# Optimization experiments

Measured on AMD Instinct MI355X. Metric: run time of the kernel, lower is better.

## Reference

```python
import math
import jax, jax.numpy as jnp
import numpy as np

N_EMBD = 1024
N_HEAD = 16
B, T = 2, 2048


def _heads(t):
    # (B, T, D) -> (B, H, T, hd)
    b, s, d = t.shape
    return t.reshape(b, s, N_HEAD, d // N_HEAD).transpose(0, 2, 1, 3)


def setup_inputs() -> dict:
    key = jax.random.key(0)
    ks = jax.random.split(key, 7)
    D = N_EMBD
    s = 0.02
    return {
        "x": jax.random.normal(ks[0], (B, T, D), dtype=jnp.float32),
        "w_attn": jax.random.normal(ks[1], (2 * D, D), dtype=jnp.float32) * s,
        "b_attn": jnp.zeros((2 * D,), dtype=jnp.float32),
        "w_k2": jax.random.normal(ks[2], (D, D), dtype=jnp.float32) * s,
        "b_k2": jnp.zeros((D,), dtype=jnp.float32),
        "w_proj": jax.random.normal(ks[3], (D, D), dtype=jnp.float32) * s,
        "b_proj": jnp.zeros((D,), dtype=jnp.float32),
    }


def reference(x, w_attn, b_attn, w_k2, b_k2, w_proj, b_proj):
    b, t, d = x.shape
    hd = d // N_HEAD
    scale = 1.0 / math.sqrt(hd)

    # QKV projections: q,k from c_attn; v is raw x reshaped into heads
    qk = x @ w_attn.T + b_attn
    q, k = jnp.split(qk, 2, axis=-1)
    q, k, v = _heads(q), _heads(k), _heads(x)  # (B,H,T,hd)

    # AR branch: standard causal softmax attention
    scores = jnp.einsum("bhqd,bhkd->bhqk", q, k) * scale
    causal = jnp.tril(jnp.ones((t, t), dtype=bool))
    scores = jnp.where(causal, scores, -jnp.inf)
    y_ar = jnp.einsum("bhqk,bhkd->bhqd", jax.nn.softmax(scores, axis=-1), v)

    # MA branch on one-step residuals e_t = v_{t+1} - y_ar_t
    e = v[:, :, 1:, :] - y_ar[:, :, :-1, :]           # (B,H,T-1,hd)
    q2 = q[:, :, 1:, :]
    k2 = _heads(x[:, :-1] @ w_k2.T + b_k2)            # (B,H,T-1,hd)

    qa = -jax.nn.leaky_relu(-q2 * scale, negative_slope=0.02)  # ma_q_activation
    ka = jax.nn.sigmoid((k2 * scale) * 0.02)                   # ma_k_activation, k=0.02

    ma = jnp.einsum("bhqd,bhkd->bhqk", qa, ka)        # (B,H,T-1,T-1), no softmax
    ma = jnp.where(jnp.tril(jnp.ones((t - 1, t - 1), dtype=bool)), ma, 0.0)
    y_ma = jnp.einsum("bhqk,bhkd->bhqd", ma, e)
    y_ma = jnp.concatenate([jnp.zeros_like(y_ma[:, :, :1, :]), y_ma], axis=2)

    def merge(z):  # (B,H,T,hd) -> (B,T,D)
        return z.transpose(0, 2, 1, 3).reshape(b, t, d)

    out = (merge(y_ar) @ w_proj.T + b_proj) + (merge(y_ma) @ w_proj.T + b_proj)
    return out
```

## Files before the change

### kernel.cpp

```cpp
#include <hip/hip_runtime.h>
#include <hip/hip_bf16.h>
#include <math.h>

#define BB  2
#define TT  2048
#define DDE 1024
#define NHH 16
#define HDD 64

typedef __bf16 bf16_t;
typedef __attribute__((ext_vector_type(8))) __bf16 bf16x8;
typedef __attribute__((ext_vector_type(4))) __bf16 bf16x4;
typedef __attribute__((ext_vector_type(4))) float  f32x4;

#define MFMA(a, b, c) __builtin_amdgcn_mfma_f32_16x16x32_bf16((a), (b), (c), 0, 0, 0)

#define WAIT_VM6()   asm volatile("s_waitcnt vmcnt(6)" ::: "memory")
#define WAIT_VM4()   asm volatile("s_waitcnt vmcnt(4)" ::: "memory")
#define WAIT_VM0()   asm volatile("s_waitcnt vmcnt(0)" ::: "memory")
#define WAIT_LGKM0() asm volatile("s_waitcnt lgkmcnt(0)" ::: "memory")

__device__ inline void wg_barrier() {
    __builtin_amdgcn_sched_barrier(0);
    __builtin_amdgcn_s_barrier();
    __builtin_amdgcn_sched_barrier(0);
}

__device__ inline unsigned int cvtpk(float a, float b) {
    unsigned int r;
    asm("v_cvt_pk_bf16_f32 %0, %1, %2" : "=v"(r) : "v"(a), "v"(b));
    return r;
}

__device__ inline float fexp2(float x) {
    float r;
    asm("v_exp_f32 %0, %1" : "=v"(r) : "v"(x));
    return r;
}

__device__ inline void pl16swap(unsigned int &a, unsigned int &b) {
    asm("v_permlane16_swap_b32 %0, %1" : "+v"(a), "+v"(b));
}

__device__ inline void gll16(const bf16_t* g, unsigned short* l) {
    __builtin_amdgcn_global_load_lds(
        (const __attribute__((address_space(1))) void*)g,
        (__attribute__((address_space(3))) void*)l, 16, 0, 0);
}

template<int ROWS, int NW = 4>
__device__ inline void stage_tile(const bf16_t* g0, size_t gstride,
                                  unsigned short* lds, int wave, int lane)
{
    const int r8 = lane >> 3;
    const int ck = (lane & 7) ^ r8;
    constexpr int RW = ROWS / NW;
    const bf16_t* g = g0 + (size_t)(wave * RW + r8) * gstride + ck * 8;
    unsigned short* l = lds + wave * RW * 64 + lane * 8;
    #pragma unroll
    for (int i = 0; i < RW / 8; ++i)
        gll16(g + (size_t)(i * 8) * gstride, l + i * 512);
}

__global__ __launch_bounds__(256) void cvt_all(
    const float* __restrict__ x, const float* __restrict__ wa,
    const float* __restrict__ wk, const float* __restrict__ wp,
    bf16_t* __restrict__ out)
{
    const size_t NX  = (size_t)BB*TT*DDE;
    const size_t NWA = (size_t)2*DDE*DDE;
    const size_t NW  = (size_t)DDE*DDE;
    const size_t e = ((size_t)blockIdx.x * 256 + threadIdx.x) * 4;
    const float* src;
    if (e < NX)                 src = x  + e;
    else if (e < NX + NWA)      src = wa + (e - NX);
    else if (e < NX + NWA + NW) src = wk + (e - NX - NWA);
    else                        src = wp + (e - NX - NWA - NW);
    float4 v = *(const float4*)src;
    bf16x4 o;
    o[0] = (bf16_t)v.x; o[1] = (bf16_t)v.y;
    o[2] = (bf16_t)v.z; o[3] = (bf16_t)v.w;
    *(bf16x4*)(out + e) = o;
}

__global__ __launch_bounds__(256) void transpose_head(
    const bf16_t* __restrict__ src, bf16_t* __restrict__ dst)
{
    const int t0 = blockIdx.x * 64, h = blockIdx.y, b = blockIdx.z;
    const int tid = threadIdx.x;
    __shared__ __align__(16) bf16_t tile[64 * 64];

    #pragma unroll
    for (int it = 0; it < 2; ++it) {
        const int t = it * 32 + (tid >> 3);
        const int cw = tid & 7;
        const int slot = (cw + (t >> 3)) & 7;
        bf16x8 v = *(const bf16x8*)(src + (size_t)(b*TT + t0 + t)*DDE + h*HDD + cw*8);
        *(bf16x8*)(tile + t*64 + slot*8) = v;
    }
    __syncthreads();
    const int bh = b * NHH + h;
    #pragma unroll
    for (int it = 0; it < 2; ++it) {
        const int d = it * 32 + (tid >> 3);
        const int co = tid & 7;
        const int slot = ((d >> 3) + co) & 7;
        bf16x8 o;
        #pragma unroll
        for (int j = 0; j < 8; ++j)
            o[j] = tile[(co*8 + j)*64 + slot*8 + (d & 7)];
        *(bf16x8*)(dst + (size_t)(bh*64 + d)*TT + t0 + co*8) = o;
    }
}

__global__ __launch_bounds__(256) void build_etg(
    const bf16_t* __restrict__ yarb, const bf16_t* __restrict__ xb,
    bf16_t* __restrict__ etg)
{
    const int t0 = blockIdx.x * 64, h = blockIdx.y, b = blockIdx.z;
    const int tid = threadIdx.x;
    const int bh = b * NHH + h;
    __shared__ __align__(16) bf16_t tile[64 * 64];

    #pragma unroll
    for (int it = 0; it < 2; ++it) {
        const int t = it * 32 + (tid >> 3);
        const int cw = tid & 7;
        const int slot = (cw + (t >> 3)) & 7;
        const int tg = t0 + t;
        bf16x8 ev;
        if (tg == 0) {
            #pragma unroll
            for (int u = 0; u < 8; ++u) ev[u] = (bf16_t)0.f;
        } else {
            bf16x8 xv = *(const bf16x8*)(xb   + (size_t)(b*TT + tg)*DDE + h*HDD + cw*8);
            bf16x8 nv = *(const bf16x8*)(yarb + (size_t)(b*TT + tg - 1)*DDE + h*HDD + cw*8);
            #pragma unroll
            for (int u = 0; u < 8; ++u)
                ev[u] = (bf16_t)((float)xv[u] - (float)nv[u]);
        }
        *(bf16x8*)(tile + t*64 + slot*8) = ev;
    }
    __syncthreads();
    #pragma unroll
    for (int it = 0; it < 2; ++it) {
        const int d = it * 32 + (tid >> 3);
        const int co = tid & 7;
        const int slot = ((d >> 3) + co) & 7;
        bf16x8 o;
        #pragma unroll
        for (int j = 0; j < 8; ++j)
            o[j] = tile[(co*8 + j)*64 + slot*8 + (d & 7)];
        *(bf16x8*)(etg + (size_t)(bh*64 + d)*TT + t0 + co*8) = o;
    }
}

__global__ __launch_bounds__(256) void gemm_qkk2(
    const bf16_t* __restrict__ A, const bf16_t* __restrict__ wab,
    const bf16_t* __restrict__ wkb, const float* __restrict__ b_attn,
    const float* __restrict__ b_k2, bf16_t* __restrict__ qkb,
    bf16_t* __restrict__ qab, bf16_t* __restrict__ kcs)
{
    __shared__ __align__(16) unsigned short As[2][64 * 64];
    __shared__ __align__(16) unsigned short Bs[2][128 * 64];
    const int tid  = threadIdx.x;
    const int wave = tid >> 6, lane = tid & 63;
    const int l15  = lane & 15, quad = lane >> 4;
    const int lid = (int)blockIdx.y * 24 + (int)blockIdx.x;
    const int s   = (lid & 7) * 192 + (lid >> 3);
    const int bm = (s / 24) * 64, bn = (s % 24) * 128;
    const int wm = (wave & 1) * 32, wn = (wave >> 1) * 64;
    const int region = bn >> 10;
    const int K = DDE;
    constexpr int NST = DDE / 64;

    const bf16_t* W = (region < 2) ? wab + (size_t)bn * K
                                   : wkb + (size_t)(bn - 2048) * K;
    const float* bp = (region < 2) ? b_attn + bn : b_k2 + (bn - 2048);
    const bf16_t* Ab = A + (size_t)bm * K;

    f32x4 acc[2][4];
    #pragma unroll
    for (int i = 0; i < 2; ++i)
        #pragma unroll
        for (int j = 0; j < 4; ++j) acc[i][j] = (f32x4)0.f;

    stage_tile<64>(Ab, K, As[0], wave, lane);
    stage_tile<128>(W,  K, Bs[0], wave, lane);
    stage_tile<64>(Ab + 64, K, As[1], wave, lane);
    stage_tile<128>(W  + 64, K, Bs[1], wave, lane);

    for (int t = 0; t < NST; ++t) {
        if (t + 1 < NST) WAIT_VM6(); else WAIT_VM0();
        wg_barrier();
        const unsigned short* Ac = As[t & 1];
        const unsigned short* Bc = Bs[t & 1];
        bf16x8 af[2][2], bfr[4][2];
        #pragma unroll
        for (int mt = 0; mt < 2; ++mt)
            #pragma unroll
            for (int kh = 0; kh < 2; ++kh)
                af[mt][kh] = *(const bf16x8*)(Ac + (wm + mt*16 + l15)*64
                                              + (((kh*4 + quad) ^ (l15 & 7))*8));
        #pragma unroll
        for (int nt = 0; nt < 4; ++nt)
            #pragma unroll
            for (int kh = 0; kh < 2; ++kh)
                bfr[nt][kh] = *(const bf16x8*)(Bc + (wn + nt*16 + l15)*64
                                               + (((kh*4 + quad) ^ (l15 & 7))*8));
        __builtin_amdgcn_s_setprio(1);
        #pragma unroll
        for (int mt = 0; mt < 2; ++mt)
            #pragma unroll
            for (int nt = 0; nt < 4; ++nt) {
                acc[mt][nt] = MFMA(af[mt][0], bfr[nt][0], acc[mt][nt]);
                acc[mt][nt] = MFMA(af[mt][1], bfr[nt][1], acc[mt][nt]);
            }
        __builtin_amdgcn_s_setprio(0);
        WAIT_LGKM0();
        wg_barrier();
        if (t + 2 < NST) {
            stage_tile<64>(Ab + (t+2)*64, K, As[t & 1], wave, lane);
            stage_tile<128>(W  + (t+2)*64, K, Bs[t & 1], wave, lane);
        }
    }

    #pragma unroll
    for (int nt = 0; nt < 4; ++nt) {
        const int cl = wn + nt*16 + l15;
        const float bj = bp[cl];
        const int cg = bn + cl;
        #pragma unroll
        for (int mt = 0; mt < 2; ++mt)
            #pragma unroll
            for (int r = 0; r < 4; ++r) {
                const int row = bm + wm + mt*16 + quad*4 + r;
                const float v = acc[mt][nt][r] + bj;
                if (region == 0) {
                    qkb[(size_t)row * (2*DDE) + cg] = (bf16_t)(v * 0.180336880f);
                    const float z = v * 0.125f;
                    qab[(size_t)row * DDE + cg] = (bf16_t)((v > 0.f) ? 0.02f*z : z);
                } else if (region == 1) {
                    qkb[(size_t)row * (2*DDE) + cg] = (bf16_t)v;
                } else {
                    const int c2 = cg - 2048;
                    const float kc = 1.f/(1.f + __expf(-v*0.0025f)) - 0.5f;
                    if (((row + 1) & (TT - 1)) != 0)
                        kcs[(size_t)(row + 1) * DDE + c2] = (bf16_t)kc;
                    if ((row & (TT - 1)) == 0)
                        kcs[(size_t)row * DDE + c2] = (bf16_t)0.f;
                }
            }
    }
}

__global__ __launch_bounds__(256) void gemm_proj(
    const bf16_t* __restrict__ A, const bf16_t* __restrict__ W,
    const float* __restrict__ bias, float* __restrict__ C,
    int M, int N, int K, float bmul)
{
    __shared__ __align__(16) unsigned short As[2][64 * 64];
    __shared__ __align__(16) unsigned short Bs[2][64 * 64];
    const int tid  = threadIdx.x;
    const int wave = tid >> 6, lane = tid & 63;
    const int l15  = lane & 15, quad = lane >> 4;
    const int lid = (int)blockIdx.y * 16 + (int)blockIdx.x;
    const int s   = (lid & 7) * 128 + (lid >> 3);
    const int bm = (s / 16) * 64, bn = (s % 16) * 64;
    const int wm = (wave & 1) * 32, wn = (wave >> 1) * 32;

    const bf16_t* Ab = A + (size_t)bm * K;
    const bf16_t* Wb = W + (size_t)bn * K;
    const int NST = K / 64;

    f32x4 acc[2][2];
    #pragma unroll
    for (int i = 0; i < 2; ++i)
        #pragma unroll
        for (int j = 0; j < 2; ++j) acc[i][j] = (f32x4)0.f;

    stage_tile<64>(Ab, K, As[0], wave, lane);
    stage_tile<64>(Wb, K, Bs[0], wave, lane);
    stage_tile<64>(Ab + 64, K, As[1], wave, lane);
    stage_tile<64>(Wb + 64, K, Bs[1], wave, lane);

    for (int t = 0; t < NST; ++t) {
        if (t + 1 < NST) WAIT_VM4(); else WAIT_VM0();
        wg_barrier();
        const unsigned short* Ac = As[t & 1];
        const unsigned short* Bc = Bs[t & 1];
        bf16x8 af[2][2], bfr[2][2];
        #pragma unroll
        for (int mt = 0; mt < 2; ++mt)
            #pragma unroll
            for (int kh = 0; kh < 2; ++kh)
                af[mt][kh] = *(const bf16x8*)(Ac + (wm + mt*16 + l15)*64
                                              + (((kh*4 + quad) ^ (l15 & 7))*8));
        #pragma unroll
        for (int nt = 0; nt < 2; ++nt)
            #pragma unroll
            for (int kh = 0; kh < 2; ++kh)
                bfr[nt][kh] = *(const bf16x8*)(Bc + (wn + nt*16 + l15)*64
                                               + (((kh*4 + quad) ^ (l15 & 7))*8));
        __builtin_amdgcn_s_setprio(1);
        #pragma unroll
        for (int mt = 0; mt < 2; ++mt)
            #pragma unroll
            for (int nt = 0; nt < 2; ++nt) {
                acc[mt][nt] = MFMA(af[mt][0], bfr[nt][0], acc[mt][nt]);
                acc[mt][nt] = MFMA(af[mt][1], bfr[nt][1], acc[mt][nt]);
            }
        __builtin_amdgcn_s_setprio(0);
        WAIT_LGKM0();
        wg_barrier();
        if (t + 2 < NST) {
            stage_tile<64>(Ab + (t+2)*64, K, As[t & 1], wave, lane);
            stage_tile<64>(Wb + (t+2)*64, K, Bs[t & 1], wave, lane);
        }
    }

    #pragma unroll
    for (int nt = 0; nt < 2; ++nt) {
        const int col = bn + wn + nt*16 + l15;
        const float bj = bias[col] * bmul;
        #pragma unroll
        for (int mt = 0; mt < 2; ++mt)
            #pragma unroll
            for (int r = 0; r < 4; ++r) {
                const int row = bm + wm + mt*16 + quad*4 + r;
                C[(size_t)row * N + col] = acc[mt][nt][r] + bj;
            }
    }
}

__global__ __launch_bounds__(512) void attn_ar_mfma(
    const bf16_t* __restrict__ qkb, const bf16_t* __restrict__ vtg,
    bf16_t* __restrict__ yarb)
{
    const int h = blockIdx.y, b = blockIdx.z;
    const int p = b ? (15 - (int)blockIdx.x) : (int)blockIdx.x;
    const int qtL = p, qtH = 31 - p;
    const int tid = threadIdx.x, wave = tid >> 6, lane = tid & 63;
    const int l15 = lane & 15, quad = lane >> 4;
    const int qt = (wave < 4) ? qtL : qtH;
    const int qw0 = qt * 64 + (wave & 3) * 16;
    const int bh = b * NHH + h;

    __shared__ __align__(16) unsigned short Ks[2][2][64 * 64];
    __shared__ __align__(16) unsigned short Vs[2][2][64 * 64];

    const int nit = qtH + 1;
    const int npair = (nit + 1) >> 1;

    const bf16_t* kg = qkb + (size_t)(b*TT)*(2*DDE) + DDE + h*HDD;
    const bf16_t* vg = vtg + (size_t)(bh*64)*TT;

    const bf16_t* qrow = qkb + (size_t)(b*TT + qw0 + l15)*(2*DDE) + h*HDD;
    bf16x8 qf[2];
    qf[0] = *(const bf16x8*)(qrow + quad*8);
    qf[1] = *(const bf16x8*)(qrow + (quad + 4)*8);

    stage_tile<64, 8>(kg, 2*DDE, Ks[0][0], wave, lane);
    stage_tile<64, 8>(vg, TT, Vs[0][0], wave, lane);
    stage_tile<64, 8>(kg + (size_t)64*(2*DDE), 2*DDE, Ks[0][1], wave, lane);
    stage_tile<64, 8>(vg + 64, TT, Vs[0][1], wave, lane);
    {
        const int t2 = min(2, nit-1), t3 = min(3, nit-1);
        stage_tile<64, 8>(kg + (size_t)t2*64*(2*DDE), 2*DDE, Ks[1][0], wave, lane);
        stage_tile<64, 8>(vg + t2*64, TT, Vs[1][0], wave, lane);
        stage_tile<64, 8>(kg + (size_t)t3*64*(2*DDE), 2*DDE, Ks[1][1], wave, lane);
        stage_tile<64, 8>(vg + t3*64, TT, Vs[1][1], wave, lane);
    }
    WAIT_VM4();
    wg_barrier();

    f32x4 o[4];
    f32x4 ls = (f32x4)0.f;
    #pragma unroll
    for (int nt = 0; nt < 4; ++nt) o[nt] = (f32x4)0.f;
    bf16x8 onesb;
    #pragma unroll
    for (int j = 0; j < 8; ++j) onesb[j] = (bf16_t)1.f;

    const int cq = ((quad & 1) << 1) | (quad >> 1);

    for (int jp = 0; jp < npair; ++jp) {
        if (jp > 0) {
            if (jp + 1 < npair) WAIT_VM4(); else WAIT_VM0();
            wg_barrier();
        }
        #pragma unroll
        for (int half = 0; half < 2; ++half) {
            const int tt = 2*jp + half;
            const int s0 = tt * 64;
            if (tt < nit && s0 <= qw0 + 31) {
                const unsigned short* Kc = Ks[jp & 1][half];
                const unsigned short* Vc = Vs[jp & 1][half];

                f32x4 sv[4];
                __builtin_amdgcn_s_setprio(1);
                #pragma unroll
                for (int nt = 0; nt < 4; ++nt) {
                    const unsigned short* kr = Kc + (nt*16 + l15)*64;
                    bf16x8 kb0 = *(const bf16x8*)(kr + ((quad    ) ^ (l15 & 7))*8);
                    bf16x8 kb1 = *(const bf16x8*)(kr + ((quad + 4) ^ (l15 & 7))*8);
                    f32x4 z = (f32x4)0.f;
                    z = MFMA(kb0, qf[0], z);
                    z = MFMA(kb1, qf[1], z);
                    sv[nt] = z;
                }
                __builtin_amdgcn_s_setprio(0);

                const bool domask = (s0 + 63 > qw0);
                const int qg = qw0 + l15;
                unsigned int pk[4][2];
                #pragma unroll
                for (int nt = 0; nt < 4; ++nt) {
                    float pv[4];
                    #pragma unroll
                    for (int r = 0; r < 4; ++r) {
                        float pe = fexp2(sv[nt][r]);
                        if (domask) {
                            const int sg = s0 + nt*16 + quad*4 + r;
                            if (sg > qg) pe = 0.f;
                        }
                        pv[r] = pe;
                    }
                    pk[nt][0] = cvtpk(pv[0], pv[1]);
                    pk[nt][1] = cvtpk(pv[2], pv[3]);
                }
                bf16x8 pa[2];
                #pragma unroll
                for (int sc = 0; sc < 2; ++sc) {
                    pl16swap(pk[2*sc][0], pk[2*sc+1][0]);
                    pl16swap(pk[2*sc][1], pk[2*sc+1][1]);
                    union { unsigned int u[4]; bf16x8 v; } pu;
                    pu.u[0] = pk[2*sc][0];
                    pu.u[1] = pk[2*sc][1];
                    pu.u[2] = pk[2*sc+1][0];
                    pu.u[3] = pk[2*sc+1][1];
                    pa[sc] = pu.v;
                }

                __builtin_amdgcn_s_setprio(1);
                ls = MFMA(pa[0], onesb, ls);
                ls = MFMA(pa[1], onesb, ls);
                #pragma unroll
                for (int nt = 0; nt < 4; ++nt) {
                    const unsigned short* vr = Vc + (nt*16 + l15)*64;
                    bf16x8 vb0 = *(const bf16x8*)(vr + ((cq    ) ^ (l15 & 7))*8);
                    bf16x8 vb1 = *(const bf16x8*)(vr + ((cq + 4) ^ (l15 & 7))*8);
                    o[nt] = MFMA(pa[0], vb0, o[nt]);
                    o[nt] = MFMA(pa[1], vb1, o[nt]);
                }
                __builtin_amdgcn_s_setprio(0);
            }
        }
        WAIT_LGKM0();
        wg_barrier();
        if (jp + 2 < npair) {
            const int t0 = 2*(jp + 2);
            const int t1 = min(t0 + 1, nit - 1);
            stage_tile<64, 8>(kg + (size_t)t0*64*(2*DDE), 2*DDE, Ks[jp & 1][0], wave, lane);
            stage_tile<64, 8>(vg + t0*64, TT, Vs[jp & 1][0], wave, lane);
            stage_tile<64, 8>(kg + (size_t)t1*64*(2*DDE), 2*DDE, Ks[jp & 1][1], wave, lane);
            stage_tile<64, 8>(vg + t1*64, TT, Vs[jp & 1][1], wave, lane);
        }
    }

    float inv[4];
    #pragma unroll
    for (int r = 0; r < 4; ++r) inv[r] = 1.f / ls[r];
    #pragma unroll
    for (int nt = 0; nt < 4; ++nt)
        #pragma unroll
        for (int r = 0; r < 4; ++r) {
            const int row = qw0 + quad*4 + r;
            const int col = h*HDD + nt*16 + l15;
            yarb[(size_t)(b*TT + row)*DDE + col] = (bf16_t)(o[nt][r] * inv[r]);
        }
}

__global__ __launch_bounds__(512) void attn_ma_mfma(
    const bf16_t* __restrict__ qab, const bf16_t* __restrict__ kcs,
    const bf16_t* __restrict__ etg, const bf16_t* __restrict__ yarb,
    bf16_t* __restrict__ ysumb)
{
    const int h = blockIdx.y, b = blockIdx.z;
    const int p = b ? (15 - (int)blockIdx.x) : (int)blockIdx.x;
    const int qtL = p, qtH = 31 - p;
    const int tid = threadIdx.x, wave = tid >> 6, lane = tid & 63;
    const int l15 = lane & 15, quad = lane >> 4;
    const int qt = (wave < 4) ? qtL : qtH;
    const int qw0 = qt * 64 + (wave & 3) * 16;
    const int bh = b * NHH + h;

    __shared__ __align__(16) unsigned short Ks[2][2][64 * 64];
    __shared__ __align__(16) unsigned short Es[2][2][64 * 64];

    const int nit = qtH + 1;
    const int npair = (nit + 1) >> 1;

    const bf16_t* kg = kcs + (size_t)(b*TT)*DDE + h*HDD;
    const bf16_t* eg = etg + (size_t)(bh*64)*TT;

    const bf16_t* qrow = qab + (size_t)(b*TT + qw0 + l15)*DDE + h*HDD;
    bf16x8 qf[2];
    qf[0] = *(const bf16x8*)(qrow + quad*8);
    qf[1] = *(const bf16x8*)(qrow + (quad + 4)*8);

    stage_tile<64, 8>(kg, DDE, Ks[0][0], wave, lane);
    stage_tile<64, 8>(eg, TT, Es[0][0], wave, lane);
    stage_tile<64, 8>(kg + (size_t)64*DDE, DDE, Ks[0][1], wave, lane);
    stage_tile<64, 8>(eg + 64, TT, Es[0][1], wave, lane);
    {
        const int t2 = min(2, nit-1), t3 = min(3, nit-1);
        stage_tile<64, 8>(kg + (size_t)t2*64*DDE, DDE, Ks[1][0], wave, lane);
        stage_tile<64, 8>(eg + t2*64, TT, Es[1][0], wave, lane);
        stage_tile<64, 8>(kg + (size_t)t3*64*DDE, DDE, Ks[1][1], wave, lane);
        stage_tile<64, 8>(eg + t3*64, TT, Es[1][1], wave, lane);
    }
    WAIT_VM4();
    wg_barrier();

    float rs = 0.f;
    #pragma unroll
    for (int kc = 0; kc < 2; ++kc)
        #pragma unroll
        for (int u = 0; u < 8; ++u) rs += (float)qf[kc][u];
    rs += __shfl_xor(rs, 16);
    rs += __shfl_xor(rs, 32);
    const float Rr = 0.5f * rs;

    f32x4 o[4];
    #pragma unroll
    for (int nt = 0; nt < 4; ++nt) o[nt] = (f32x4)0.f;

    const int cq = ((quad & 1) << 1) | (quad >> 1);

    for (int jp = 0; jp < npair; ++jp) {
        if (jp > 0) {
            if (jp + 1 < npair) WAIT_VM4(); else WAIT_VM0();
            wg_barrier();
        }
        #pragma unroll
        for (int half = 0; half < 2; ++half) {
            const int tt = 2*jp + half;
            const int s0 = tt * 64;
            if (tt < nit && s0 <= qw0 + 31) {
                const unsigned short* Kc = Ks[jp & 1][half];
                const unsigned short* Ec = Es[jp & 1][half];

                f32x4 sv[4];
                __builtin_amdgcn_s_setprio(1);
                #pragma unroll
                for (int nt = 0; nt < 4; ++nt) {
                    const unsigned short* kr = Kc + (nt*16 + l15)*64;
                    bf16x8 kb0 = *(const bf16x8*)(kr + ((quad    ) ^ (l15 & 7))*8);
                    bf16x8 kb1 = *(const bf16x8*)(kr + ((quad + 4) ^ (l15 & 7))*8);
                    f32x4 z = (f32x4)0.f;
                    z = MFMA(kb0, qf[0], z);
                    z = MFMA(kb1, qf[1], z);
                    sv[nt] = z;
                }
                __builtin_amdgcn_s_setprio(0);

                const bool domask = (s0 + 63 > qw0);
                const bool m0 = (tt == 0);
                const int qg = qw0 + l15;
                unsigned int pk[4][2];
                #pragma unroll
                for (int nt = 0; nt < 4; ++nt) {
                    float pv[4];
                    #pragma unroll
                    for (int r = 0; r < 4; ++r) {
                        const int sg = s0 + nt*16 + quad*4 + r;
                        float pe = sv[nt][r] + Rr;
                        if (m0 && sg == 0) pe = 0.f;
                        if (domask && sg > qg) pe = 0.f;
                        pv[r] = pe;
                    }
                    pk[nt][0] = cvtpk(pv[0], pv[1]);
                    pk[nt][1] = cvtpk(pv[2], pv[3]);
                }
                bf16x8 pa[2];
                #pragma unroll
                for (int sc = 0; sc < 2; ++sc) {
                    pl16swap(pk[2*sc][0], pk[2*sc+1][0]);
                    pl16swap(pk[2*sc][1], pk[2*sc+1][1]);
                    union { unsigned int u[4]; bf16x8 v; } pu;
                    pu.u[0] = pk[2*sc][0];
                    pu.u[1] = pk[2*sc][1];
                    pu.u[2] = pk[2*sc+1][0];
                    pu.u[3] = pk[2*sc+1][1];
                    pa[sc] = pu.v;
                }

                __builtin_amdgcn_s_setprio(1);
                #pragma unroll
                for (int nt = 0; nt < 4; ++nt) {
                    const unsigned short* er = Ec + (nt*16 + l15)*64;
                    bf16x8 eb0 = *(const bf16x8*)(er + ((cq    ) ^ (l15 & 7))*8);
                    bf16x8 eb1 = *(const bf16x8*)(er + ((cq + 4) ^ (l15 & 7))*8);
                    o[nt] = MFMA(pa[0], eb0, o[nt]);
                    o[nt] = MFMA(pa[1], eb1, o[nt]);
                }
                __builtin_amdgcn_s_setprio(0);
            }
        }
        WAIT_LGKM0();
        wg_barrier();
        if (jp + 2 < npair) {
            const int t0 = 2*(jp + 2);
            const int t1 = min(t0 + 1, nit - 1);
            stage_tile<64, 8>(kg + (size_t)t0*64*DDE, DDE, Ks[jp & 1][0], wave, lane);
            stage_tile<64, 8>(eg + t0*64, TT, Es[jp & 1][0], wave, lane);
            stage_tile<64, 8>(kg + (size_t)t1*64*DDE, DDE, Ks[jp & 1][1], wave, lane);
            stage_tile<64, 8>(eg + t1*64, TT, Es[jp & 1][1], wave, lane);
        }
    }

    #pragma unroll
    for (int nt = 0; nt < 4; ++nt)
        #pragma unroll
        for (int r = 0; r < 4; ++r) {
            const int row = qw0 + quad*4 + r;
            const int col = h*HDD + nt*16 + l15;
            const size_t e = (size_t)(b*TT + row)*DDE + col;
            ysumb[e] = (bf16_t)((float)yarb[e] + o[nt][r]);
        }
}

extern "C" void kernel_launch(void* const* d_in, const int* in_sizes, int n_in,
                              void* d_out, int out_size, void* d_ws, size_t ws_size,
                              hipStream_t stream)
{
    const float* x      = (const float*)d_in[0];
    const float* w_attn = (const float*)d_in[1];
    const float* b_attn = (const float*)d_in[2];
    const float* w_k2   = (const float*)d_in[3];
    const float* b_k2   = (const float*)d_in[4];
    const float* w_proj = (const float*)d_in[5];
    const float* b_proj = (const float*)d_in[6];

    const size_t NX  = (size_t)BB*TT*DDE;
    const size_t NWA = (size_t)2*DDE*DDE;
    const size_t NW  = (size_t)DDE*DDE;
    const size_t NQK = (size_t)BB*TT*2*DDE;

    bf16_t* xb   = (bf16_t*)d_ws;
    bf16_t* wab  = xb   + NX;
    bf16_t* wkb  = wab  + NWA;
    bf16_t* wpb  = wkb  + NW;
    bf16_t* qkb  = wpb  + NW;
    bf16_t* qab  = qkb  + NQK;
    bf16_t* kcs  = qab  + NX;
    bf16_t* vtg  = kcs  + NX;
    bf16_t* ysumb= vtg  + NX;
    bf16_t* yarb = (bf16_t*)((float*)(vtg + NX) + NX);
    bf16_t* etg  = vtg;

    const size_t NCVT = NX + NWA + NW + NW;
    cvt_all<<<NCVT / 1024, 256, 0, stream>>>(x, w_attn, w_k2, w_proj, xb);

    transpose_head<<<dim3(TT/64, NHH, BB), 256, 0, stream>>>(xb, vtg);

    const int M = BB * TT;
    gemm_qkk2<<<dim3(24, M/64), 256, 0, stream>>>(xb, wab, wkb, b_attn, b_k2,
                                                   qkb, qab, kcs);

    attn_ar_mfma<<<dim3(16, NHH, BB), 512, 0, stream>>>(qkb, vtg, yarb);
    build_etg<<<dim3(TT/64, NHH, BB), 256, 0, stream>>>(yarb, xb, etg);
    attn_ma_mfma<<<dim3(16, NHH, BB), 512, 0, stream>>>(qab, kcs, etg, yarb, ysumb);

    gemm_proj<<<dim3(DDE/64, M/64), 256, 0, stream>>>(ysumb, wpb, b_proj,
                                                      (float*)d_out, M, DDE, DDE, 2.f);
}
```

Measured before the change: 229.3 us.

## Split KV tiles across wave halves in attention kernels, reduce partials via LDS

Both attention kernels change how work is split inside a block. Before, waves 0-3 handled the low query tile and waves 4-7 the high query tile, so the two halves carried unequal causal work. Now each wave half takes alternate KV tiles and computes both query tiles, which balances the load. Partial outputs and row sums are combined through LDS at the end. This adds register pressure from double accumulators, an extra reduction barrier, and a launch_bounds occupancy hint.

```diff
diff --git a/kernel.cpp b/kernel.cpp
--- a/kernel.cpp
+++ b/kernel.cpp
@@ -333,7 +333,63 @@
     }
 }
 
-__global__ __launch_bounds__(512) void attn_ar_mfma(
+#define AR_UNIT(QF, OO, LSACC, QW0)  do {                                   \
+    f32x4 sv[4];                                                            \
+    __builtin_amdgcn_s_setprio(1);                                          \
+    _Pragma("unroll")                                                       \
+    for (int nt = 0; nt < 4; ++nt) {                                        \
+        const unsigned short* kr = Kc + (nt*16 + l15)*64;                   \
+        bf16x8 kb0 = *(const bf16x8*)(kr + ((quad    ) ^ (l15 & 7))*8);     \
+        bf16x8 kb1 = *(const bf16x8*)(kr + ((quad + 4) ^ (l15 & 7))*8);     \
+        f32x4 z = (f32x4)0.f;                                               \
+        z = MFMA(kb0, QF[0], z);                                            \
+        z = MFMA(kb1, QF[1], z);                                            \
+        sv[nt] = z;                                                         \
+    }                                                                       \
+    __builtin_amdgcn_s_setprio(0);                                          \
+    const bool domask = (s0 + 63 > (QW0));                                  \
+    const int qg = (QW0) + l15;                                             \
+    unsigned int pk[4][2];                                                  \
+    _Pragma("unroll")                                                       \
+    for (int nt = 0; nt < 4; ++nt) {                                        \
+        float pv[4];                                                        \
+        _Pragma("unroll")                                                   \
+        for (int r = 0; r < 4; ++r) {                                       \
+            float pe = fexp2(sv[nt][r]);                                    \
+            if (domask) {                                                   \
+                const int sg = s0 + nt*16 + quad*4 + r;                     \
+                if (sg > qg) pe = 0.f;                                      \
+            }                                                               \
+            pv[r] = pe;                                                     \
+        }                                                                   \
+        pk[nt][0] = cvtpk(pv[0], pv[1]);                                    \
+        pk[nt][1] = cvtpk(pv[2], pv[3]);                                    \
+    }                                                                       \
+    bf16x8 pa[2];                                                           \
+    _Pragma("unroll")                                                       \
+    for (int sc = 0; sc < 2; ++sc) {                                        \
+        pl16swap(pk[2*sc][0], pk[2*sc+1][0]);                               \
+        pl16swap(pk[2*sc][1], pk[2*sc+1][1]);                               \
+        union { unsigned int uu[4]; bf16x8 v; } pu;                         \
+        pu.uu[0] = pk[2*sc][0];   pu.uu[1] = pk[2*sc][1];                   \
+        pu.uu[2] = pk[2*sc+1][0]; pu.uu[3] = pk[2*sc+1][1];                 \
+        pa[sc] = pu.v;                                                      \
+    }                                                                       \
+    __builtin_amdgcn_s_setprio(1);                                          \
+    LSACC = MFMA(pa[0], onesb, LSACC);                                      \
+    LSACC = MFMA(pa[1], onesb, LSACC);                                      \
+    _Pragma("unroll")                                                       \
+    for (int nt = 0; nt < 4; ++nt) {                                        \
+        const unsigned short* vr = Vc + (nt*16 + l15)*64;                   \
+        bf16x8 vb0 = *(const bf16x8*)(vr + ((cq    ) ^ (l15 & 7))*8);       \
+        bf16x8 vb1 = *(const bf16x8*)(vr + ((cq + 4) ^ (l15 & 7))*8);       \
+        OO[nt] = MFMA(pa[0], vb0, OO[nt]);                                  \
+        OO[nt] = MFMA(pa[1], vb1, OO[nt]);                                  \
+    }                                                                       \
+    __builtin_amdgcn_s_setprio(0);                                          \
+} while (0)
+
+__global__ __launch_bounds__(512, 4) void attn_ar_mfma(
     const bf16_t* __restrict__ qkb, const bf16_t* __restrict__ vtg,
     bf16_t* __restrict__ yarb)
 {
@@ -342,12 +398,12 @@
     const int qtL = p, qtH = 31 - p;
     const int tid = threadIdx.x, wave = tid >> 6, lane = tid & 63;
     const int l15 = lane & 15, quad = lane >> 4;
-    const int qt = (wave < 4) ? qtL : qtH;
-    const int qw0 = qt * 64 + (wave & 3) * 16;
+    const int wl = wave & 3, wsid = wave >> 2;
+    const int qw0L = qtL * 64 + wl * 16;
+    const int qw0H = qtH * 64 + wl * 16;
     const int bh = b * NHH + h;
 
-    __shared__ __align__(16) unsigned short Ks[2][2][64 * 64];
-    __shared__ __align__(16) unsigned short Vs[2][2][64 * 64];
+    __shared__ __align__(16) unsigned short Lds[2][2][2][64 * 64];
 
     const int nit = qtH + 1;
     const int npair = (nit + 1) >> 1;
@@ -355,29 +411,30 @@
     const bf16_t* kg = qkb + (size_t)(b*TT)*(2*DDE) + DDE + h*HDD;
     const bf16_t* vg = vtg + (size_t)(bh*64)*TT;
 
-    const bf16_t* qrow = qkb + (size_t)(b*TT + qw0 + l15)*(2*DDE) + h*HDD;
-    bf16x8 qf[2];
-    qf[0] = *(const bf16x8*)(qrow + quad*8);
-    qf[1] = *(const bf16x8*)(qrow + (quad + 4)*8);
-
-    stage_tile<64, 8>(kg, 2*DDE, Ks[0][0], wave, lane);
-    stage_tile<64, 8>(vg, TT, Vs[0][0], wave, lane);
-    stage_tile<64, 8>(kg + (size_t)64*(2*DDE), 2*DDE, Ks[0][1], wave, lane);
-    stage_tile<64, 8>(vg + 64, TT, Vs[0][1], wave, lane);
-    {
-        const int t2 = min(2, nit-1), t3 = min(3, nit-1);
-        stage_tile<64, 8>(kg + (size_t)t2*64*(2*DDE), 2*DDE, Ks[1][0], wave, lane);
-        stage_tile<64, 8>(vg + t2*64, TT, Vs[1][0], wave, lane);
-        stage_tile<64, 8>(kg + (size_t)t3*64*(2*DDE), 2*DDE, Ks[1][1], wave, lane);
-        stage_tile<64, 8>(vg + t3*64, TT, Vs[1][1], wave, lane);
-    }
+    const bf16_t* qrowL = qkb + (size_t)(b*TT + qw0L + l15)*(2*DDE) + h*HDD;
+    const bf16_t* qrowH = qkb + (size_t)(b*TT + qw0H + l15)*(2*DDE) + h*HDD;
+    bf16x8 qfL[2], qfH[2];
+    qfL[0] = *(const bf16x8*)(qrowL + quad*8);
+    qfL[1] = *(const bf16x8*)(qrowL + (quad + 4)*8);
+    qfH[0] = *(const bf16x8*)(qrowH + quad*8);
+    qfH[1] = *(const bf16x8*)(qrowH + (quad + 4)*8);
+    __builtin_amdgcn_sched_barrier(0);
+
+    stage_tile<64, 8>(kg, 2*DDE, &Lds[0][0][0][0], wave, lane);
+    stage_tile<64, 8>(vg, TT,    &Lds[0][0][1][0], wave, lane);
+    stage_tile<64, 8>(kg + (size_t)64*(2*DDE), 2*DDE, &Lds[0][1][0][0], wave, lane);
+    stage_tile<64, 8>(vg + 64, TT, &Lds[0][1][1][0], wave, lane);
+    stage_tile<64, 8>(kg + (size_t)2*64*(2*DDE), 2*DDE, &Lds[1][0][0][0], wave, lane);
+    stage_tile<64, 8>(vg + 2*64, TT, &Lds[1][0][1][0], wave, lane);
+    stage_tile<64, 8>(kg + (size_t)3*64*(2*DDE), 2*DDE, &Lds[1][1][0][0], wave, lane);
+    stage_tile<64, 8>(vg + 3*64, TT, &Lds[1][1][1][0], wave, lane);
     WAIT_VM4();
     wg_barrier();
 
-    f32x4 o[4];
-    f32x4 ls = (f32x4)0.f;
-    #pragma unroll
-    for (int nt = 0; nt < 4; ++nt) o[nt] = (f32x4)0.f;
+    f32x4 oH[4], oL[4];
+    f32x4 lsH = (f32x4)0.f, lsL = (f32x4)0.f;
+    #pragma unroll
+    for (int nt = 0; nt < 4; ++nt) { oH[nt] = (f32x4)0.f; oL[nt] = (f32x4)0.f; }
     bf16x8 onesb;
     #pragma unroll
     for (int j = 0; j < 8; ++j) onesb[j] = (bf16_t)1.f;
@@ -389,99 +446,119 @@
             if (jp + 1 < npair) WAIT_VM4(); else WAIT_VM0();
             wg_barrier();
         }
-        #pragma unroll
-        for (int half = 0; half < 2; ++half) {
-            const int tt = 2*jp + half;
-            const int s0 = tt * 64;
-            if (tt < nit && s0 <= qw0 + 31) {
-                const unsigned short* Kc = Ks[jp & 1][half];
-                const unsigned short* Vc = Vs[jp & 1][half];
-
-                f32x4 sv[4];
-                __builtin_amdgcn_s_setprio(1);
-                #pragma unroll
-                for (int nt = 0; nt < 4; ++nt) {
-                    const unsigned short* kr = Kc + (nt*16 + l15)*64;
-                    bf16x8 kb0 = *(const bf16x8*)(kr + ((quad    ) ^ (l15 & 7))*8);
-                    bf16x8 kb1 = *(const bf16x8*)(kr + ((quad + 4) ^ (l15 & 7))*8);
-                    f32x4 z = (f32x4)0.f;
-                    z = MFMA(kb0, qf[0], z);
-                    z = MFMA(kb1, qf[1], z);
-                    sv[nt] = z;
-                }
-                __builtin_amdgcn_s_setprio(0);
-
-                const bool domask = (s0 + 63 > qw0);
-                const int qg = qw0 + l15;
-                unsigned int pk[4][2];
-                #pragma unroll
-                for (int nt = 0; nt < 4; ++nt) {
-                    float pv[4];
-                    #pragma unroll
-                    for (int r = 0; r < 4; ++r) {
-                        float pe = fexp2(sv[nt][r]);
-                        if (domask) {
-                            const int sg = s0 + nt*16 + quad*4 + r;
-                            if (sg > qg) pe = 0.f;
-                        }
-                        pv[r] = pe;
-                    }
-                    pk[nt][0] = cvtpk(pv[0], pv[1]);
-                    pk[nt][1] = cvtpk(pv[2], pv[3]);
-                }
-                bf16x8 pa[2];
-                #pragma unroll
-                for (int sc = 0; sc < 2; ++sc) {
-                    pl16swap(pk[2*sc][0], pk[2*sc+1][0]);
-                    pl16swap(pk[2*sc][1], pk[2*sc+1][1]);
-                    union { unsigned int u[4]; bf16x8 v; } pu;
-                    pu.u[0] = pk[2*sc][0];
-                    pu.u[1] = pk[2*sc][1];
-                    pu.u[2] = pk[2*sc+1][0];
-                    pu.u[3] = pk[2*sc+1][1];
-                    pa[sc] = pu.v;
-                }
-
-                __builtin_amdgcn_s_setprio(1);
-                ls = MFMA(pa[0], onesb, ls);
-                ls = MFMA(pa[1], onesb, ls);
-                #pragma unroll
-                for (int nt = 0; nt < 4; ++nt) {
-                    const unsigned short* vr = Vc + (nt*16 + l15)*64;
-                    bf16x8 vb0 = *(const bf16x8*)(vr + ((cq    ) ^ (l15 & 7))*8);
-                    bf16x8 vb1 = *(const bf16x8*)(vr + ((cq + 4) ^ (l15 & 7))*8);
-                    o[nt] = MFMA(pa[0], vb0, o[nt]);
-                    o[nt] = MFMA(pa[1], vb1, o[nt]);
-                }
-                __builtin_amdgcn_s_setprio(0);
-            }
-        }
+        const int myt = 2*jp + wsid;
+        const int s0 = myt * 64;
+        const unsigned short* Kc = &Lds[jp & 1][wsid][0][0];
+        const unsigned short* Vc = &Lds[jp & 1][wsid][1][0];
+
+        if (myt <= qtH) AR_UNIT(qfH, oH, lsH, qw0H);
+        if (myt <= p)   AR_UNIT(qfL, oL, lsL, qw0L);
+
         WAIT_LGKM0();
         wg_barrier();
         if (jp + 2 < npair) {
             const int t0 = 2*(jp + 2);
             const int t1 = min(t0 + 1, nit - 1);
-            stage_tile<64, 8>(kg + (size_t)t0*64*(2*DDE), 2*DDE, Ks[jp & 1][0], wave, lane);
-            stage_tile<64, 8>(vg + t0*64, TT, Vs[jp & 1][0], wave, lane);
-            stage_tile<64, 8>(kg + (size_t)t1*64*(2*DDE), 2*DDE, Ks[jp & 1][1], wave, lane);
-            stage_tile<64, 8>(vg + t1*64, TT, Vs[jp & 1][1], wave, lane);
-        }
-    }
-
+            stage_tile<64, 8>(kg + (size_t)t0*64*(2*DDE), 2*DDE, &Lds[jp & 1][0][0][0], wave, lane);
+            stage_tile<64, 8>(vg + t0*64, TT, &Lds[jp & 1][0][1][0], wave, lane);
+            stage_tile<64, 8>(kg + (size_t)t1*64*(2*DDE), 2*DDE, &Lds[jp & 1][1][0][0], wave, lane);
+            stage_tile<64, 8>(vg + t1*64, TT, &Lds[jp & 1][1][1][0], wave, lane);
+        }
+    }
+
+    float* S = (float*)&Lds[0][0][0][0];
+    float* my = S + (size_t)(wave*64 + lane)*20;
+    {
+        const f32x4 (&os)[4] = wsid ? oL : oH;
+        const f32x4 &lss     = wsid ? lsL : lsH;
+        #pragma unroll
+        for (int nt = 0; nt < 4; ++nt)
+            #pragma unroll
+            for (int r = 0; r < 4; ++r) my[nt*4 + r] = os[nt][r];
+        #pragma unroll
+        for (int r = 0; r < 4; ++r) my[16 + r] = lss[r];
+    }
+    WAIT_LGKM0();
+    wg_barrier();
+    const float* peer = S + (size_t)((wave ^ 4)*64 + lane)*20;
+    f32x4 (&ok)[4] = wsid ? oH : oL;
+    f32x4 &lsk     = wsid ? lsH : lsL;
+    #pragma unroll
+    for (int nt = 0; nt < 4; ++nt)
+        #pragma unroll
+        for (int r = 0; r < 4; ++r) ok[nt][r] += peer[nt*4 + r];
+    #pragma unroll
+    for (int r = 0; r < 4; ++r) lsk[r] += peer[16 + r];
+
+    const int qt = wsid ? qtH : qtL;
     float inv[4];
     #pragma unroll
-    for (int r = 0; r < 4; ++r) inv[r] = 1.f / ls[r];
+    for (int r = 0; r < 4; ++r) inv[r] = 1.f / lsk[r];
     #pragma unroll
     for (int nt = 0; nt < 4; ++nt)
         #pragma unroll
         for (int r = 0; r < 4; ++r) {
-            const int row = qw0 + quad*4 + r;
+            const int row = qt*64 + wl*16 + quad*4 + r;
             const int col = h*HDD + nt*16 + l15;
-            yarb[(size_t)(b*TT + row)*DDE + col] = (bf16_t)(o[nt][r] * inv[r]);
-        }
-}
-
-__global__ __launch_bounds__(512) void attn_ma_mfma(
+            yarb[(size_t)(b*TT + row)*DDE + col] = (bf16_t)(ok[nt][r] * inv[r]);
+        }
+}
+
+#define MA_UNIT(QF, OO, RR, QW0)  do {                                      \
+    f32x4 sv[4];                                                            \
+    __builtin_amdgcn_s_setprio(1);                                          \
+    _Pragma("unroll")                                                       \
+    for (int nt = 0; nt < 4; ++nt) {                                        \
+        const unsigned short* kr = Kc + (nt*16 + l15)*64;                   \
+        bf16x8 kb0 = *(const bf16x8*)(kr + ((quad    ) ^ (l15 & 7))*8);     \
+        bf16x8 kb1 = *(const bf16x8*)(kr + ((quad + 4) ^ (l15 & 7))*8);     \
+        f32x4 z = (f32x4)0.f;                                               \
+        z = MFMA(kb0, QF[0], z);                                            \
+        z = MFMA(kb1, QF[1], z);                                            \
+        sv[nt] = z;                                                         \
+    }                                                                       \
+    __builtin_amdgcn_s_setprio(0);                                          \
+    const bool domask = (s0 + 63 > (QW0));                                  \
+    const bool m0 = (myt == 0);                                             \
+    const int qg = (QW0) + l15;                                             \
+    unsigned int pk[4][2];                                                  \
+    _Pragma("unroll")                                                       \
+    for (int nt = 0; nt < 4; ++nt) {                                        \
+        float pv[4];                                                        \
+        _Pragma("unroll")                                                   \
+        for (int r = 0; r < 4; ++r) {                                       \
+            const int sg = s0 + nt*16 + quad*4 + r;                         \
+            float pe = sv[nt][r] + (RR);                                    \
+            if (m0 && sg == 0) pe = 0.f;                                    \
+            if (domask && sg > qg) pe = 0.f;                                \
+            pv[r] = pe;                                                     \
+        }                                                                   \
+        pk[nt][0] = cvtpk(pv[0], pv[1]);                                    \
+        pk[nt][1] = cvtpk(pv[2], pv[3]);                                    \
+    }                                                                       \
+    bf16x8 pa[2];                                                           \
+    _Pragma("unroll")                                                       \
+    for (int sc = 0; sc < 2; ++sc) {                                        \
+        pl16swap(pk[2*sc][0], pk[2*sc+1][0]);                               \
+        pl16swap(pk[2*sc][1], pk[2*sc+1][1]);                               \
+        union { unsigned int uu[4]; bf16x8 v; } pu;                         \
+        pu.uu[0] = pk[2*sc][0];   pu.uu[1] = pk[2*sc][1];                   \
+        pu.uu[2] = pk[2*sc+1][0]; pu.uu[3] = pk[2*sc+1][1];                 \
+        pa[sc] = pu.v;                                                      \
+    }                                                                       \
+    __builtin_amdgcn_s_setprio(1);                                          \
+    _Pragma("unroll")                                                       \
+    for (int nt = 0; nt < 4; ++nt) {                                        \
+        const unsigned short* er = Vc + (nt*16 + l15)*64;                   \
+        bf16x8 eb0 = *(const bf16x8*)(er + ((cq    ) ^ (l15 & 7))*8);       \
+        bf16x8 eb1 = *(const bf16x8*)(er + ((cq + 4) ^ (l15 & 7))*8);       \
+        OO[nt] = MFMA(pa[0], eb0, OO[nt]);                                  \
+        OO[nt] = MFMA(pa[1], eb1, OO[nt]);                                  \
+    }                                                                       \
+    __builtin_amdgcn_s_setprio(0);                                          \
+} while (0)
+
+__global__ __launch_bounds__(512, 4) void attn_ma_mfma(
     const bf16_t* __restrict__ qab, const bf16_t* __restrict__ kcs,
     const bf16_t* __restrict__ etg, const bf16_t* __restrict__ yarb,
     bf16_t* __restrict__ ysumb)
@@ -491,12 +568,12 @@
     const int qtL = p, qtH = 31 - p;
     const int tid = threadIdx.x, wave = tid >> 6, lane = tid & 63;
     const int l15 = lane & 15, quad = lane >> 4;
-    const int qt = (wave < 4) ? qtL : qtH;
-    const int qw0 = qt * 64 + (wave & 3) * 16;
+    const int wl = wave & 3, wsid = wave >> 2;
+    const int qw0L = qtL * 64 + wl * 16;
+    const int qw0H = qtH * 64 + wl * 16;
     const int bh = b * NHH + h;
 
-    __shared__ __align__(16) unsigned short Ks[2][2][64 * 64];
-    __shared__ __align__(16) unsigned short Es[2][2][64 * 64];
+    __shared__ __align__(16) unsigned short Lds[2][2][2][64 * 64];
 
     const int nit = qtH + 1;
     const int npair = (nit + 1) >> 1;
@@ -504,37 +581,39 @@
     const bf16_t* kg = kcs + (size_t)(b*TT)*DDE + h*HDD;
     const bf16_t* eg = etg + (size_t)(bh*64)*TT;
 
-    const bf16_t* qrow = qab + (size_t)(b*TT + qw0 + l15)*DDE + h*HDD;
-    bf16x8 qf[2];
-    qf[0] = *(const bf16x8*)(qrow + quad*8);
-    qf[1] = *(const bf16x8*)(qrow + (quad + 4)*8);
-
-    stage_tile<64, 8>(kg, DDE, Ks[0][0], wave, lane);
-    stage_tile<64, 8>(eg, TT, Es[0][0], wave, lane);
-    stage_tile<64, 8>(kg + (size_t)64*DDE, DDE, Ks[0][1], wave, lane);
-    stage_tile<64, 8>(eg + 64, TT, Es[0][1], wave, lane);
-    {
-        const int t2 = min(2, nit-1), t3 = min(3, nit-1);
-        stage_tile<64, 8>(kg + (size_t)t2*64*DDE, DDE, Ks[1][0], wave, lane);
-        stage_tile<64, 8>(eg + t2*64, TT, Es[1][0], wave, lane);
-        stage_tile<64, 8>(kg + (size_t)t3*64*DDE, DDE, Ks[1][1], wave, lane);
-        stage_tile<64, 8>(eg + t3*64, TT, Es[1][1], wave, lane);
-    }
+    const bf16_t* qrowL = qab + (size_t)(b*TT + qw0L + l15)*DDE + h*HDD;
+    const bf16_t* qrowH = qab + (size_t)(b*TT + qw0H + l15)*DDE + h*HDD;
+    bf16x8 qfL[2], qfH[2];
+    qfL[0] = *(const bf16x8*)(qrowL + quad*8);
+    qfL[1] = *(const bf16x8*)(qrowL + (quad + 4)*8);
+    qfH[0] = *(const bf16x8*)(qrowH + quad*8);
+    qfH[1] = *(const bf16x8*)(qrowH + (quad + 4)*8);
+    __builtin_amdgcn_sched_barrier(0);
+
+    stage_tile<64, 8>(kg, DDE, &Lds[0][0][0][0], wave, lane);
+    stage_tile<64, 8>(eg, TT,  &Lds[0][0][1][0], wave, lane);
+    stage_tile<64, 8>(kg + (size_t)64*DDE, DDE, &Lds[0][1][0][0], wave, lane);
+    stage_tile<64, 8>(eg + 64, TT, &Lds[0][1][1][0], wave, lane);
+    stage_tile<64, 8>(kg + (size_t)2*64*DDE, DDE, &Lds[1][0][0][0], wave, lane);
+    stage_tile<64, 8>(eg + 2*64, TT, &Lds[1][0][1][0], wave, lane);
+    stage_tile<64, 8>(kg + (size_t)3*64*DDE, DDE, &Lds[1][1][0][0], wave, lane);
+    stage_tile<64, 8>(eg + 3*64, TT, &Lds[1][1][1][0], wave, lane);
     WAIT_VM4();
     wg_barrier();
 
-    float rs = 0.f;
+    float rsL = 0.f, rsH = 0.f;
     #pragma unroll
     for (int kc = 0; kc < 2; ++kc)
         #pragma unroll
-        for (int u = 0; u < 8; ++u) rs += (float)qf[kc][u];
-    rs += __shfl_xor(rs, 16);
-    rs += __shfl_xor(rs, 32);
-    const float Rr = 0.5f * rs;
-
-    f32x4 o[4];
-    #pragma unroll
-    for (int nt = 0; nt < 4; ++nt) o[nt] = (f32x4)0.f;
+        for (int u = 0; u < 8; ++u) { rsL += (float)qfL[kc][u]; rsH += (float)qfH[kc][u]; }
+    rsL += __shfl_xor(rsL, 16); rsL += __shfl_xor(rsL, 32);
+    rsH += __shfl_xor(rsH, 16); rsH += __shfl_xor(rsH, 32);
+    const float RrL = 0.5f * rsL;
+    const float RrH = 0.5f * rsH;
+
+    f32x4 oH[4], oL[4];
+    #pragma unroll
+    for (int nt = 0; nt < 4; ++nt) { oH[nt] = (f32x4)0.f; oL[nt] = (f32x4)0.f; }
 
     const int cq = ((quad & 1) << 1) | (quad >> 1);
 
@@ -543,91 +622,53 @@
             if (jp + 1 < npair) WAIT_VM4(); else WAIT_VM0();
             wg_barrier();
         }
-        #pragma unroll
-        for (int half = 0; half < 2; ++half) {
-            const int tt = 2*jp + half;
-            const int s0 = tt * 64;
-            if (tt < nit && s0 <= qw0 + 31) {
-                const unsigned short* Kc = Ks[jp & 1][half];
-                const unsigned short* Ec = Es[jp & 1][half];
-
-                f32x4 sv[4];
-                __builtin_amdgcn_s_setprio(1);
-                #pragma unroll
-                for (int nt = 0; nt < 4; ++nt) {
-                    const unsigned short* kr = Kc + (nt*16 + l15)*64;
-                    bf16x8 kb0 = *(const bf16x8*)(kr + ((quad    ) ^ (l15 & 7))*8);
-                    bf16x8 kb1 = *(const bf16x8*)(kr + ((quad + 4) ^ (l15 & 7))*8);
-                    f32x4 z = (f32x4)0.f;
-                    z = MFMA(kb0, qf[0], z);
-                    z = MFMA(kb1, qf[1], z);
-                    sv[nt] = z;
-                }
-                __builtin_amdgcn_s_setprio(0);
-
-                const bool domask = (s0 + 63 > qw0);
-                const bool m0 = (tt == 0);
-                const int qg = qw0 + l15;
-                unsigned int pk[4][2];
-                #pragma unroll
-                for (int nt = 0; nt < 4; ++nt) {
-                    float pv[4];
-                    #pragma unroll
-                    for (int r = 0; r < 4; ++r) {
-                        const int sg = s0 + nt*16 + quad*4 + r;
-                        float pe = sv[nt][r] + Rr;
-                        if (m0 && sg == 0) pe = 0.f;
-                        if (domask && sg > qg) pe = 0.f;
-                        pv[r] = pe;
-                    }
-                    pk[nt][0] = cvtpk(pv[0], pv[1]);
-                    pk[nt][1] = cvtpk(pv[2], pv[3]);
-                }
-                bf16x8 pa[2];
-                #pragma unroll
-                for (int sc = 0; sc < 2; ++sc) {
-                    pl16swap(pk[2*sc][0], pk[2*sc+1][0]);
-                    pl16swap(pk[2*sc][1], pk[2*sc+1][1]);
-                    union { unsigned int u[4]; bf16x8 v; } pu;
-                    pu.u[0] = pk[2*sc][0];
-                    pu.u[1] = pk[2*sc][1];
-                    pu.u[2] = pk[2*sc+1][0];
-                    pu.u[3] = pk[2*sc+1][1];
-                    pa[sc] = pu.v;
-                }
-
-                __builtin_amdgcn_s_setprio(1);
-                #pragma unroll
-                for (int nt = 0; nt < 4; ++nt) {
-                    const unsigned short* er = Ec + (nt*16 + l15)*64;
-                    bf16x8 eb0 = *(const bf16x8*)(er + ((cq    ) ^ (l15 & 7))*8);
-                    bf16x8 eb1 = *(const bf16x8*)(er + ((cq + 4) ^ (l15 & 7))*8);
-                    o[nt] = MFMA(pa[0], eb0, o[nt]);
-                    o[nt] = MFMA(pa[1], eb1, o[nt]);
-                }
-                __builtin_amdgcn_s_setprio(0);
-            }
-        }
+        const int myt = 2*jp + wsid;
+        const int s0 = myt * 64;
+        const unsigned short* Kc = &Lds[jp & 1][wsid][0][0];
+        const unsigned short* Vc = &Lds[jp & 1][wsid][1][0];
+
+        if (myt <= qtH) MA_UNIT(qfH, oH, RrH, qw0H);
+        if (myt <= p)   MA_UNIT(qfL, oL, RrL, qw0L);
+
         WAIT_LGKM0();
         wg_barrier();
         if (jp + 2 < npair) {
             const int t0 = 2*(jp + 2);
             const int t1 = min(t0 + 1, nit - 1);
-            stage_tile<64, 8>(kg + (size_t)t0*64*DDE, DDE, Ks[jp & 1][0], wave, lane);
-            stage_tile<64, 8>(eg + t0*64, TT, Es[jp & 1][0], wave, lane);
-            stage_tile<64, 8>(kg + (size_t)t1*64*DDE, DDE, Ks[jp & 1][1], wave, lane);
-            stage_tile<64, 8>(eg + t1*64, TT, Es[jp & 1][1], wave, lane);
-        }
-    }
-
+            stage_tile<64, 8>(kg + (size_t)t0*64*DDE, DDE, &Lds[jp & 1][0][0][0], wave, lane);
+            stage_tile<64, 8>(eg + t0*64, TT, &Lds[jp & 1][0][1][0], wave, lane);
+            stage_tile<64, 8>(kg + (size_t)t1*64*DDE, DDE, &Lds[jp & 1][1][0][0], wave, lane);
+            stage_tile<64, 8>(eg + t1*64, TT, &Lds[jp & 1][1][1][0], wave, lane);
+        }
+    }
+
+    float* S = (float*)&Lds[0][0][0][0];
+    float* my = S + (size_t)(wave*64 + lane)*16;
+    {
+        const f32x4 (&os)[4] = wsid ? oL : oH;
+        #pragma unroll
+        for (int nt = 0; nt < 4; ++nt)
+            #pragma unroll
+            for (int r = 0; r < 4; ++r) my[nt*4 + r] = os[nt][r];
+    }
+    WAIT_LGKM0();
+    wg_barrier();
+    const float* peer = S + (size_t)((wave ^ 4)*64 + lane)*16;
+    f32x4 (&ok)[4] = wsid ? oH : oL;
     #pragma unroll
     for (int nt = 0; nt < 4; ++nt)
         #pragma unroll
+        for (int r = 0; r < 4; ++r) ok[nt][r] += peer[nt*4 + r];
+
+    const int qt = wsid ? qtH : qtL;
+    #pragma unroll
+    for (int nt = 0; nt < 4; ++nt)
+        #pragma unroll
         for (int r = 0; r < 4; ++r) {
-            const int row = qw0 + quad*4 + r;
+            const int row = qt*64 + wl*16 + quad*4 + r;
             const int col = h*HDD + nt*16 + l15;
             const size_t e = (size_t)(b*TT + row)*DDE + col;
-            ysumb[e] = (bf16_t)((float)yarb[e] + o[nt][r]);
+            ysumb[e] = (bf16_t)((float)yarb[e] + ok[nt][r]);
         }
 }
 
```

Measured after the change: 216.9 us (median of 3 runs). -5.4%, faster.
